# Kernel optimization log

Hardware: AMD Instinct MI355X
Metric: run time of the kernel (lower is better)

The kernel has to match this reference:

```python
import jax, jax.numpy as jnp
import numpy as np

L, T, F, DIM = 16, 16384, 2, 3
N_MIN, N_MAX = 16.0, 512.0
N_PTS = 262144
# torch code builds np.int32 primes [1, 2654435761, 805459861]; 2654435761 wraps to -1640531535.
# Since T is a power of two, int32 wraparound multiply/xor followed by nonnegative mod T gives
# bit-identical indices to the int64 torch computation.
PIS = jnp.array([1, -1640531535, 805459861], dtype=jnp.int32)
# corner ordering from get_indices: corner k = a*4+b*2+c with a->dim0, b->dim1, c->dim2
OFFS = jnp.array([[(k >> 2) & 1, (k >> 1) & 1, k & 1] for k in range(8)], dtype=jnp.float32)  # (8,3)


def setup_inputs() -> dict:
    key = jax.random.key(0)
    k1, k2 = jax.random.split(key)
    x = jax.random.uniform(k1, (N_PTS, DIM), dtype=jnp.float32)
    # nn.init.uniform_(weight, a=-1e-4, b=1e-4) for each of L tables of shape (T, F)
    embeddings = jax.random.uniform(k2, (L, T, F), minval=-1e-4, maxval=1e-4, dtype=jnp.float32)
    return {"x": x, "embeddings": embeddings}


def reference(x, embeddings):
    # per-level growth factor b = exp((log Nmax - log Nmin)/L); N_l = Nmin * b**l
    b = jnp.exp((jnp.log(N_MAX) - jnp.log(N_MIN)) / L)
    N_l = N_MIN * b ** jnp.arange(L, dtype=jnp.float32)                      # (L,)
    un_x = x[None, :, :] * N_l[:, None, None]                                # (L,N,3)  (mu=0, sigma=1)
    lo = jnp.floor(un_x)
    hi = jnp.ceil(un_x)
    d = hi - lo                                                              # (L,N,3)
    nz = d != 0
    diff = jnp.where(nz, (un_x - lo) / jnp.where(nz, d, 1.0), 0.0)           # (L,N,3)

    mask = OFFS.astype(bool)[None, None]                                     # (1,1,8,3)
    corners = jnp.where(mask, hi[:, :, None, :], lo[:, :, None, :])          # (L,N,8,3)
    ci = corners.astype(jnp.int32)
    prod = ci * PIS                                                          # (L,N,8,3) wrapping int32 mul
    idx = jnp.mod(prod[..., 0] ^ prod[..., 1] ^ prod[..., 2], T)             # (L,N,8)

    # per-level table gather: (L,T,F)[ (L,N,8) ] -> (L,N,8,F)
    feats = jax.vmap(lambda emb, i: emb[i])(embeddings, idx)

    # trilinear weights: prod over dims of (diff if corner bit else 1-diff)
    w = jnp.prod(jnp.where(mask, diff[:, :, None, :], 1.0 - diff[:, :, None, :]), axis=-1)  # (L,N,8)
    c = jnp.einsum('lnc,lncf->lnf', w, feats)                                # (L,N,F)
    return jnp.transpose(c, (1, 0, 2)).reshape(x.shape[0], L * F)            # (N, L*F)
```

## Files before the change

kernel.cpp:

```cpp
#include <hip/hip_runtime.h>
#include <stdint.h>

constexpr int L_LEVELS = 16;
constexpr int T_SIZE   = 16384;
constexpr int N_PTS    = 262144;

typedef _Float16 h2 __attribute__((ext_vector_type(2)));
typedef _Float16 h4 __attribute__((ext_vector_type(4)));

template <bool DIRECT>
__global__ __launch_bounds__(1024, 8) void hash_encode_lds(
    const float* __restrict__ x,
    const float* __restrict__ emb,
    void* __restrict__ dst_raw)
{
    __shared__ __align__(16) h2 tab[T_SIZE];

    const int l     = blockIdx.x & (L_LEVELS - 1);
    const int chunk = blockIdx.x >> 4;
    const int t     = threadIdx.x;
    const int base  = chunk * 8192;

    {
        const float4* __restrict__ src =
            reinterpret_cast<const float4*>(emb + (size_t)l * T_SIZE * 2);
        h4* __restrict__ d4 = reinterpret_cast<h4*>(tab);
#pragma unroll
        for (int it = 0; it < 8; ++it) {
            const int i = it * 1024 + t;
            float4 v = src[i];
            h4 w = { (_Float16)v.x, (_Float16)v.y,
                     (_Float16)v.z, (_Float16)v.w };
            d4[i] = w;
        }
    }
    __syncthreads();

    const float Nl = 16.0f * exp2f((float)l * 0.3125f);

#pragma unroll 2
    for (int p = 0; p < 8; ++p) {
        const int n = base + p * 1024 + t;

        const float u0 = x[n * 3 + 0] * Nl;
        const float u1 = x[n * 3 + 1] * Nl;
        const float u2 = x[n * 3 + 2] * Nl;

        const float fl0 = floorf(u0), fl1 = floorf(u1), fl2 = floorf(u2);
        const float ce0 = ceilf(u0),  ce1 = ceilf(u1),  ce2 = ceilf(u2);
        const float df0 = (ce0 != fl0) ? (u0 - fl0) : 0.0f;
        const float df1 = (ce1 != fl1) ? (u1 - fl1) : 0.0f;
        const float df2 = (ce2 != fl2) ? (u2 - fl2) : 0.0f;

        const uint32_t p0l = (uint32_t)(int32_t)fl0;
        const uint32_t p0h = (uint32_t)(int32_t)ce0;
        const uint32_t p1l = (uint32_t)(int32_t)fl1 * 2654435761u;
        const uint32_t p1h = (uint32_t)(int32_t)ce1 * 2654435761u;
        const uint32_t p2l = (uint32_t)(int32_t)fl2 * 805459861u;
        const uint32_t p2h = (uint32_t)(int32_t)ce2 * 805459861u;

        h2 f[8];
#pragma unroll
        for (int k = 0; k < 8; ++k) {
            uint32_t h = ((k & 4) ? p0h : p0l)
                       ^ ((k & 2) ? p1h : p1l)
                       ^ ((k & 1) ? p2h : p2l);
            f[k] = tab[h & (T_SIZE - 1)];
        }

        float acc0 = 0.0f, acc1 = 0.0f;
#pragma unroll
        for (int k = 0; k < 8; ++k) {
            const float w = ((k & 4) ? df0 : 1.0f - df0)
                          * ((k & 2) ? df1 : 1.0f - df1)
                          * ((k & 1) ? df2 : 1.0f - df2);
            acc0 += w * (float)f[k].x;
            acc1 += w * (float)f[k].y;
        }

        if (DIRECT) {
            float2* out = reinterpret_cast<float2*>(dst_raw);
            out[(size_t)n * L_LEVELS + l] = make_float2(acc0, acc1);
        } else {
            h2* ws = reinterpret_cast<h2*>(dst_raw);
            h2 r = { (_Float16)acc0, (_Float16)acc1 };
            ws[(size_t)l * N_PTS + n] = r;
        }
    }
}

__global__ __launch_bounds__(256) void transpose_lnf_nlf(
    const h2* __restrict__ ws,
    float2* __restrict__ out)
{
    __shared__ h2 tile[L_LEVELS][257];
    const int t    = threadIdx.x;
    const int base = blockIdx.x * 256;

#pragma unroll
    for (int l = 0; l < L_LEVELS; ++l)
        tile[l][t] = ws[(size_t)l * N_PTS + base + t];
    __syncthreads();

#pragma unroll
    for (int i = 0; i < L_LEVELS; ++i) {
        const int flat = i * 256 + t;
        const int p = flat >> 4;
        const int l = flat & 15;
        h2 v = tile[l][p];
        out[(size_t)base * L_LEVELS + flat] =
            make_float2((float)v.x, (float)v.y);
    }
}

extern "C" void kernel_launch(void* const* d_in, const int* in_sizes, int n_in,
                              void* d_out, int out_size, void* d_ws, size_t ws_size,
                              hipStream_t stream) {
    const float* x   = (const float*)d_in[0];
    const float* emb = (const float*)d_in[1];

    const size_t ws_needed = (size_t)N_PTS * L_LEVELS * sizeof(h2);

    if (ws_size >= ws_needed) {
        hash_encode_lds<false><<<512, 1024, 0, stream>>>(x, emb, d_ws);
        transpose_lnf_nlf<<<N_PTS / 256, 256, 0, stream>>>((const h2*)d_ws,
                                                           (float2*)d_out);
    } else {
        hash_encode_lds<true><<<512, 1024, 0, stream>>>(x, emb, d_out);
    }
}
```

Before: 87.56 us.

## Use incremental Gray-code hashing, fp16 trilinear lerps, and smaller blocks

The hash encoder now computes byte offsets once, then walks the 8 corners in Gray-code order, flipping one dimension's XOR delta per step instead of rehashing each corner. Interpolation becomes a chain of packed fp16 lerps replacing eight float weight products, and the ceil-based degenerate-cell handling is dropped because the fractional part is already zero in that case. Blocks shrink from 1024 to 512 threads with twice as many blocks, and the table fill uses 16-byte LDS stores. The aim is to cut integer and FP ALU work per point, at the cost of fp16 rounding in the weights and accumulation plus twice the table-fill traffic into LDS.

New measurement: 87.99 us. About the same (+0.5%).

```diff
diff --git a/kernel.cpp b/kernel.cpp
--- a/kernel.cpp
+++ b/kernel.cpp
@@ -6,85 +6,94 @@
 constexpr int N_PTS    = 262144;
 
 typedef _Float16 h2 __attribute__((ext_vector_type(2)));
-typedef _Float16 h4 __attribute__((ext_vector_type(4)));
+typedef _Float16 h8 __attribute__((ext_vector_type(8)));
+
+constexpr uint32_t P1_4 = 2654435761u * 4u;
+constexpr uint32_t P2_4 = 805459861u * 4u;
+constexpr uint32_t M4   = (T_SIZE - 1) * 4u;
+
+__device__ __forceinline__ h2 lerp2(h2 a, h2 b, h2 t) {
+    return a + t * (b - a);
+}
 
 template <bool DIRECT>
-__global__ __launch_bounds__(1024, 8) void hash_encode_lds(
+__global__ __launch_bounds__(512, 4) void hash_encode_lds(
     const float* __restrict__ x,
     const float* __restrict__ emb,
     void* __restrict__ dst_raw)
 {
-    __shared__ __align__(16) h2 tab[T_SIZE];
+    __shared__ h2 tab[T_SIZE];
 
     const int l     = blockIdx.x & (L_LEVELS - 1);
     const int chunk = blockIdx.x >> 4;
     const int t     = threadIdx.x;
-    const int base  = chunk * 8192;
+    const int base  = chunk * 4096;
 
     {
         const float4* __restrict__ src =
             reinterpret_cast<const float4*>(emb + (size_t)l * T_SIZE * 2);
-        h4* __restrict__ d4 = reinterpret_cast<h4*>(tab);
+        h8* __restrict__ d8 = reinterpret_cast<h8*>(tab);
 #pragma unroll
         for (int it = 0; it < 8; ++it) {
-            const int i = it * 1024 + t;
-            float4 v = src[i];
-            h4 w = { (_Float16)v.x, (_Float16)v.y,
-                     (_Float16)v.z, (_Float16)v.w };
-            d4[i] = w;
+            const int i = it * 512 + t;
+            float4 a = src[2 * i];
+            float4 b = src[2 * i + 1];
+            h8 w = { (_Float16)a.x, (_Float16)a.y, (_Float16)a.z, (_Float16)a.w,
+                     (_Float16)b.x, (_Float16)b.y, (_Float16)b.z, (_Float16)b.w };
+            d8[i] = w;
         }
     }
     __syncthreads();
 
     const float Nl = 16.0f * exp2f((float)l * 0.3125f);
+    const char* __restrict__ tb = reinterpret_cast<const char*>(tab);
 
 #pragma unroll 2
     for (int p = 0; p < 8; ++p) {
-        const int n = base + p * 1024 + t;
+        const int n = base + p * 512 + t;
 
         const float u0 = x[n * 3 + 0] * Nl;
         const float u1 = x[n * 3 + 1] * Nl;
         const float u2 = x[n * 3 + 2] * Nl;
 
         const float fl0 = floorf(u0), fl1 = floorf(u1), fl2 = floorf(u2);
-        const float ce0 = ceilf(u0),  ce1 = ceilf(u1),  ce2 = ceilf(u2);
-        const float df0 = (ce0 != fl0) ? (u0 - fl0) : 0.0f;
-        const float df1 = (ce1 != fl1) ? (u1 - fl1) : 0.0f;
-        const float df2 = (ce2 != fl2) ? (u2 - fl2) : 0.0f;
+        const float df0 = u0 - fl0, df1 = u1 - fl1, df2 = u2 - fl2;
 
-        const uint32_t p0l = (uint32_t)(int32_t)fl0;
-        const uint32_t p0h = (uint32_t)(int32_t)ce0;
-        const uint32_t p1l = (uint32_t)(int32_t)fl1 * 2654435761u;
-        const uint32_t p1h = (uint32_t)(int32_t)ce1 * 2654435761u;
-        const uint32_t p2l = (uint32_t)(int32_t)fl2 * 805459861u;
-        const uint32_t p2h = (uint32_t)(int32_t)ce2 * 805459861u;
+        const uint32_t q0 = ((uint32_t)(int32_t)fl0) << 2;
+        const uint32_t q1 = ((uint32_t)(int32_t)fl1) * P1_4;
+        const uint32_t q2 = ((uint32_t)(int32_t)fl2) * P2_4;
+        const uint32_t d0 = (q0 ^ (q0 + 4u))   & M4;
+        const uint32_t d1 = (q1 ^ (q1 + P1_4)) & M4;
+        const uint32_t d2 = (q2 ^ (q2 + P2_4)) & M4;
 
+        uint32_t off = (q0 ^ q1 ^ q2) & M4;
+
+        constexpr int gray[8] = {0, 1, 3, 2, 6, 7, 5, 4};
         h2 f[8];
 #pragma unroll
-        for (int k = 0; k < 8; ++k) {
-            uint32_t h = ((k & 4) ? p0h : p0l)
-                       ^ ((k & 2) ? p1h : p1l)
-                       ^ ((k & 1) ? p2h : p2l);
-            f[k] = tab[h & (T_SIZE - 1)];
+        for (int j = 0; j < 8; ++j) {
+            f[gray[j]] = *reinterpret_cast<const h2*>(tb + off);
+            if (j < 7) {
+                const int tog = gray[j] ^ gray[j + 1];
+                off ^= (tog == 4) ? d0 : (tog == 2) ? d1 : d2;
+            }
         }
 
-        float acc0 = 0.0f, acc1 = 0.0f;
-#pragma unroll
-        for (int k = 0; k < 8; ++k) {
-            const float w = ((k & 4) ? df0 : 1.0f - df0)
-                          * ((k & 2) ? df1 : 1.0f - df1)
-                          * ((k & 1) ? df2 : 1.0f - df2);
-            acc0 += w * (float)f[k].x;
-            acc1 += w * (float)f[k].y;
-        }
+        const _Float16 h0 = (_Float16)df0, h1 = (_Float16)df1, h2v = (_Float16)df2;
+        const h2 t0 = {h0, h0}, t1 = {h1, h1}, t2 = {h2v, h2v};
+        h2 e0 = lerp2(f[0], f[1], t2);
+        h2 e1 = lerp2(f[2], f[3], t2);
+        h2 e2 = lerp2(f[4], f[5], t2);
+        h2 e3 = lerp2(f[6], f[7], t2);
+        h2 g0 = lerp2(e0, e1, t1);
+        h2 g1 = lerp2(e2, e3, t1);
+        h2 r  = lerp2(g0, g1, t0);
 
         if (DIRECT) {
             float2* out = reinterpret_cast<float2*>(dst_raw);
-            out[(size_t)n * L_LEVELS + l] = make_float2(acc0, acc1);
+            out[(size_t)n * L_LEVELS + l] = make_float2((float)r.x, (float)r.y);
         } else {
-            h2* ws = reinterpret_cast<h2*>(dst_raw);
-            h2 r = { (_Float16)acc0, (_Float16)acc1 };
-            ws[(size_t)l * N_PTS + n] = r;
+            reinterpret_cast<h2*>(dst_raw)[(size_t)l * N_PTS + n] = r;
         }
     }
 }
@@ -122,10 +131,10 @@
     const size_t ws_needed = (size_t)N_PTS * L_LEVELS * sizeof(h2);
 
     if (ws_size >= ws_needed) {
-        hash_encode_lds<false><<<512, 1024, 0, stream>>>(x, emb, d_ws);
+        hash_encode_lds<false><<<1024, 512, 0, stream>>>(x, emb, d_ws);
         transpose_lnf_nlf<<<N_PTS / 256, 256, 0, stream>>>((const h2*)d_ws,
                                                            (float2*)d_out);
     } else {
-        hash_encode_lds<true><<<512, 1024, 0, stream>>>(x, emb, d_out);
+        hash_encode_lds<true><<<1024, 512, 0, stream>>>(x, emb, d_out);
     }
 }
```
